# Kernel optimization log

Measured on AMD Instinct MI355X. Metric: run time of the kernel, lower is better.

Reference implementation:

```python
import jax, jax.numpy as jnp
import numpy as np

FEATS = 1024
HEAD = 16
MLP_HIDDEN = 4096
HEAD_DIM = FEATS // HEAD
SQRT_D = float(FEATS) ** 0.5  # module scales by sqrt(feats), not sqrt(head_dim)
LN_EPS = 1e-5


def layer_norm(x, g, b):
    mu = jnp.mean(x, axis=-1, keepdims=True)
    var = jnp.mean(jnp.square(x - mu), axis=-1, keepdims=True)
    return (x - mu) * jax.lax.rsqrt(var + LN_EPS) * g + b


def setup_inputs() -> dict:
    key = jax.random.key(0)
    ks = jax.random.split(key, 12)
    s = 1.0 / np.sqrt(FEATS)
    s2 = 1.0 / np.sqrt(MLP_HIDDEN)
    return {
        "x": jax.random.normal(ks[0], (2, 2048, FEATS), dtype=jnp.float32),
        "ln1_g": jnp.ones((FEATS,), jnp.float32),
        "ln1_b": jnp.zeros((FEATS,), jnp.float32),
        "wq": jax.random.normal(ks[1], (FEATS, FEATS), jnp.float32) * s,
        "bq": jnp.zeros((FEATS,), jnp.float32),
        "wk": jax.random.normal(ks[2], (FEATS, FEATS), jnp.float32) * s,
        "bk": jnp.zeros((FEATS,), jnp.float32),
        "wv": jax.random.normal(ks[3], (FEATS, FEATS), jnp.float32) * s,
        "bv": jnp.zeros((FEATS,), jnp.float32),
        "wo": jax.random.normal(ks[4], (FEATS, FEATS), jnp.float32) * s,
        "bo": jnp.zeros((FEATS,), jnp.float32),
        "ln2_g": jnp.ones((FEATS,), jnp.float32),
        "ln2_b": jnp.zeros((FEATS,), jnp.float32),
        "w1": jax.random.normal(ks[5], (MLP_HIDDEN, FEATS), jnp.float32) * s,
        "b1": jnp.zeros((MLP_HIDDEN,), jnp.float32),
        "w2": jax.random.normal(ks[6], (FEATS, MLP_HIDDEN), jnp.float32) * s2,
        "b2": jnp.zeros((FEATS,), jnp.float32),
    }


def reference(x, ln1_g, ln1_b, wq, bq, wk, bk, wv, bv, wo, bo,
              ln2_g, ln2_b, w1, b1, w2, b2):
    b, n, f = x.shape
    h = layer_norm(x, ln1_g, ln1_b)
    # qkv projections (torch Linear: y = x @ W.T + b)
    q = (h @ wq.T + bq).reshape(b, n, HEAD, HEAD_DIM).transpose(0, 2, 1, 3)
    k = (h @ wk.T + bk).reshape(b, n, HEAD, HEAD_DIM).transpose(0, 2, 1, 3)
    v = (h @ wv.T + bv).reshape(b, n, HEAD, HEAD_DIM).transpose(0, 2, 1, 3)
    score = jax.nn.softmax(jnp.einsum('bhif,bhjf->bhij', q, k) / SQRT_D, axis=-1)
    attn = jnp.einsum('bhij,bhjf->bihf', score, v).reshape(b, n, f)
    o = attn @ wo.T + bo
    out1 = o + x
    h2 = layer_norm(out1, ln2_g, ln2_b)
    mlp = jax.nn.relu(jax.nn.relu(h2 @ w1.T + b1) @ w2.T + b2)
    return mlp + out1
```

## Files before the change

### kernel.cpp

```cpp
#include <hip/hip_runtime.h>
#include <hip/hip_bf16.h>

#define FEATS 1024
#define NH 16
#define HD 64
#define SEQ 2048
#define BATCH 2
#define MTOT (BATCH*SEQ)
#define MLPH 4096

typedef __attribute__((ext_vector_type(8))) short bf16x8;
typedef __attribute__((ext_vector_type(4))) short bf16x4;
typedef __attribute__((ext_vector_type(4))) float f32x4;

static_assert(sizeof(bf16x8) == 16, "bf16x8 must be 16B");

__device__ __forceinline__ unsigned short f2bf(float f) {
    unsigned int u = __float_as_uint(f);
    unsigned int lsb = (u >> 16) & 1u;
    u += 0x7fffu + lsb;
    return (unsigned short)(u >> 16);
}

#define ASYNC16(GP, LP) __builtin_amdgcn_global_load_lds( \
    (const __attribute__((address_space(1))) void*)(GP),  \
    (__attribute__((address_space(3))) void*)(LP), 16, 0, 0)

__global__ __launch_bounds__(256) void cvt_kernel(const float* __restrict__ src,
                                                  unsigned short* __restrict__ dst, int n) {
    int i = (blockIdx.x * 256 + threadIdx.x) * 4;
    if (i + 3 < n) {
        float4 v = *(const float4*)(src + i);
        ushort4 o;
        o.x = f2bf(v.x); o.y = f2bf(v.y); o.z = f2bf(v.z); o.w = f2bf(v.w);
        *(ushort4*)(dst + i) = o;
    }
}

__global__ __launch_bounds__(256) void concat3_kernel(const float* __restrict__ a,
                                                      const float* __restrict__ b,
                                                      const float* __restrict__ c,
                                                      float* __restrict__ o) {
    int i = blockIdx.x * 256 + threadIdx.x;
    float v = (i < 1024) ? a[i] : ((i < 2048) ? b[i - 1024] : c[i - 2048]);
    o[i] = v;
}

__global__ __launch_bounds__(256) void ln_kernel(const float* __restrict__ x,
                                                 const float* __restrict__ g,
                                                 const float* __restrict__ bta,
                                                 unsigned short* __restrict__ h) {
    __shared__ float red[8];
    const int row = blockIdx.x;
    const int t = threadIdx.x;
    const float* xr = x + (size_t)row * FEATS;
    float4 v = ((const float4*)xr)[t];
    float s  = v.x + v.y + v.z + v.w;
    float ss = v.x * v.x + v.y * v.y + v.z * v.z + v.w * v.w;
#pragma unroll
    for (int off = 1; off < 64; off <<= 1) {
        s  += __shfl_xor(s, off);
        ss += __shfl_xor(ss, off);
    }
    const int w = t >> 6;
    if ((t & 63) == 0) { red[w] = s; red[4 + w] = ss; }
    __syncthreads();
    s  = red[0] + red[1] + red[2] + red[3];
    ss = red[4] + red[5] + red[6] + red[7];
    const float mu  = s * (1.f / FEATS);
    const float var = ss * (1.f / FEATS) - mu * mu;
    const float rs  = rsqrtf(var + 1e-5f);
    float4 gv = ((const float4*)g)[t];
    float4 bv = ((const float4*)bta)[t];
    ushort4 ov;
    ov.x = f2bf((v.x - mu) * rs * gv.x + bv.x);
    ov.y = f2bf((v.y - mu) * rs * gv.y + bv.y);
    ov.z = f2bf((v.z - mu) * rs * gv.z + bv.z);
    ov.w = f2bf((v.w - mu) * rs * gv.w + bv.w);
    ((ushort4*)h)[(size_t)row * (FEATS / 4) + t] = ov;
}

template <bool RELU, bool ADD, bool OUTBF16>
__global__ __launch_bounds__(256, 3)
void gemm_kernel(const unsigned short* __restrict__ A,
                 const unsigned short* __restrict__ W,
                 const float* __restrict__ bias,
                 const float* __restrict__ addend,
                 void* __restrict__ outp,
                 int M, int N, int K, int gx) {
    __shared__ unsigned short lds[3][2][128 * 32];

    const int t = threadIdx.x;
    const int w = t >> 6, lane = t & 63;
    const int wr = w >> 1, wc = w & 1;
    const int li = lane & 15, lj = lane >> 4;

    const int nwg = gridDim.x;
    const int cpx = nwg >> 3;
    const int wg = blockIdx.x;
    const int swz = (wg & 7) * cpx + (wg >> 3);
    const int mb = (swz / gx) * 128, nb = (swz % gx) * 128;

    const int srow = lane >> 2, sc = (lane & 3) * 8;
    const unsigned short* gA = A + (size_t)(mb + w * 16 + srow) * K + sc;
    const unsigned short* gB = W + (size_t)(nb + w * 16 + srow) * K + sc;
    const size_t half = (size_t)64 * K;
    const int lbase = w * 512 + lane * 8;

    const int nt = K >> 5;

#define STAGE(BUF, K0)                                             \
    do {                                                           \
        unsigned short* la_ = &lds[BUF][0][lbase];                 \
        unsigned short* lb_ = &lds[BUF][1][lbase];                 \
        ASYNC16(gA + (K0), la_);                                   \
        ASYNC16(gA + half + (K0), la_ + 2048);                     \
        ASYNC16(gB + (K0), lb_);                                   \
        ASYNC16(gB + half + (K0), lb_ + 2048);                     \
    } while (0)

    STAGE(0, 0);
    STAGE(1, 32);
    asm volatile("s_waitcnt vmcnt(4)" ::: "memory");
    __builtin_amdgcn_s_barrier();

    f32x4 acc[4][4] = {};

    for (int i = 0; i < nt; ++i) {
        const int cur = i % 3;
        const unsigned short* Al = &lds[cur][0][0];
        const unsigned short* Bl = &lds[cur][1][0];

        bf16x8 af[4], bfr[4];
#pragma unroll
        for (int m = 0; m < 4; m++)
            af[m] = *(const bf16x8*)(Al + (wr * 64 + m * 16 + li) * 32 + lj * 8);
#pragma unroll
        for (int n = 0; n < 4; n++)
            bfr[n] = *(const bf16x8*)(Bl + (wc * 64 + n * 16 + li) * 32 + lj * 8);

        const int pf = i + 2 < nt;
        if (pf) STAGE((i + 2) % 3, (i + 2) * 32);

#pragma unroll
        for (int m = 0; m < 4; m++)
#pragma unroll
            for (int n = 0; n < 4; n++)
                acc[m][n] = __builtin_amdgcn_mfma_f32_16x16x32_bf16(af[m], bfr[n], acc[m][n], 0, 0, 0);

        if (i + 1 < nt) {
            if (pf) asm volatile("s_waitcnt vmcnt(4)" ::: "memory");
            else    asm volatile("s_waitcnt vmcnt(0)" ::: "memory");
            __builtin_amdgcn_s_barrier();
        }
    }
#undef STAGE

#pragma unroll
    for (int m = 0; m < 4; m++) {
#pragma unroll
        for (int n = 0; n < 4; n++) {
            const int col = nb + wc * 64 + n * 16 + li;
            const float bv = bias[col];
#pragma unroll
            for (int r = 0; r < 4; r++) {
                const int row = mb + wr * 64 + m * 16 + lj * 4 + r;
                float v = acc[m][n][r] + bv;
                if (RELU) v = fmaxf(v, 0.f);
                if (ADD)  v += addend[(size_t)row * N + col];
                if (OUTBF16)
                    ((unsigned short*)outp)[(size_t)row * N + col] = f2bf(v);
                else
                    ((float*)outp)[(size_t)row * N + col] = v;
            }
        }
    }
}

__global__ __launch_bounds__(256) void vtrans_kernel(const unsigned short* __restrict__ qkv,
                                                     unsigned short* __restrict__ vt) {
    constexpr int LDV = 68;
    __shared__ unsigned short Vl[64 * LDV];
    const int bh = blockIdx.x, st = blockIdx.y;
    const int b = bh >> 4, h = bh & 15;
    const int t = threadIdx.x;
    const unsigned short* src = qkv + (size_t)(b * SEQ + st * 64) * (3 * FEATS) + 2 * FEATS + h * HD;
#pragma unroll
    for (int i = 0; i < 2; i++) {
        int idx = t + i * 256;
        int r = idx >> 3, c = (idx & 7) * 8;
        *(bf16x8*)(Vl + r * LDV + c) = *(const bf16x8*)(src + (size_t)r * (3 * FEATS) + c);
    }
    __syncthreads();
    unsigned short* dst = vt + (size_t)bh * HD * SEQ + st * 64;
#pragma unroll
    for (int i = 0; i < 2; i++) {
        int idx = t + i * 256;
        int d = idx >> 3, s8 = (idx & 7) * 8;
        bf16x8 v;
#pragma unroll
        for (int j = 0; j < 8; j++) v[j] = Vl[(s8 + j) * LDV + d];
        *(bf16x8*)(dst + (size_t)d * SEQ + s8) = v;
    }
}

__global__ __launch_bounds__(512, 4)
void attn_kernel(const unsigned short* __restrict__ qkv,
                 const unsigned short* __restrict__ vt,
                 unsigned short* __restrict__ out) {
    constexpr int LK = 72;
    __shared__ unsigned short Kl[2][64 * LK];
    __shared__ unsigned short Vtl[2][64 * LK];

    const int bh = blockIdx.x;
    const int b = bh >> 4, h = bh & 15;
    const int q0 = blockIdx.y * 128;
    const int t = threadIdx.x, w = t >> 6, lane = t & 63;
    const int li = lane & 15, lj = lane >> 4;

    const size_t rstr = 3 * FEATS;
    const unsigned short* qkvb = qkv + (size_t)(b * SEQ) * rstr;
    const unsigned short* ksrc = qkvb + FEATS + h * HD;
    const unsigned short* vsrc = vt + (size_t)bh * HD * SEQ;

    bf16x8 aq[2];
#pragma unroll
    for (int kk = 0; kk < 2; kk++)
        aq[kk] = *(const bf16x8*)(qkvb + (size_t)(q0 + w * 16 + li) * rstr + h * HD + kk * 32 + lj * 8);

    f32x4 o[4] = {};
    float lsum = 0.f;
    const float c2 = 1.4426950408889634f / 32.0f;

    const int sr = t >> 3, scol = (t & 7) * 8;
    const unsigned short* kg = ksrc + (size_t)sr * rstr + scol;
    const unsigned short* vg = vsrc + (size_t)sr * SEQ + scol;
    const int ldoK = sr * LK + scol;
    const int posA = (scol & 32) + ((scol & 8) << 1) + ((scol & 16) >> 2);
    const int ldoV = sr * LK + posA;

    const int nt = SEQ / 64;

    {
        bf16x8 k0 = *(const bf16x8*)kg;
        bf16x8 v0 = *(const bf16x8*)vg;
        *(bf16x8*)(&Kl[0][ldoK]) = k0;
        bf16x4 vlo = __builtin_shufflevector(v0, v0, 0, 1, 2, 3);
        bf16x4 vhi = __builtin_shufflevector(v0, v0, 4, 5, 6, 7);
        *(bf16x4*)(&Vtl[0][ldoV])     = vlo;
        *(bf16x4*)(&Vtl[0][ldoV + 8]) = vhi;
    }

    int cur = 0;
    for (int i = 0; i < nt; ++i) {
        bf16x8 kreg, vreg;
        if (i + 1 < nt) {
            kreg = *(const bf16x8*)(kg + (size_t)(i + 1) * 64 * rstr);
            vreg = *(const bf16x8*)(vg + (i + 1) * 64);
        }

        asm volatile("s_waitcnt lgkmcnt(0)" ::: "memory");
        __builtin_amdgcn_s_barrier();

        const unsigned short* Kc = Kl[cur];
        const unsigned short* Vc = Vtl[cur];

        f32x4 s[4];
        __builtin_amdgcn_s_setprio(1);
#pragma unroll
        for (int n = 0; n < 4; n++) {
            bf16x8 k0 = *(const bf16x8*)(Kc + (n * 16 + li) * LK + lj * 8);
            bf16x8 k1 = *(const bf16x8*)(Kc + (n * 16 + li) * LK + 32 + lj * 8);
            f32x4 acc = {};
            acc = __builtin_amdgcn_mfma_f32_16x16x32_bf16(k0, aq[0], acc, 0, 0, 0);
            acc = __builtin_amdgcn_mfma_f32_16x16x32_bf16(k1, aq[1], acc, 0, 0, 0);
            s[n] = acc;
        }
        __builtin_amdgcn_s_setprio(0);

        float p[4][4];
#pragma unroll
        for (int n = 0; n < 4; n++)
#pragma unroll
            for (int r = 0; r < 4; r++) {
                p[n][r] = exp2f(s[n][r] * c2);
                lsum += p[n][r];
            }
        union { unsigned u[4]; bf16x8 v; } A0u, A1u;
#pragma unroll
        for (int n = 0; n < 2; n++) {
            asm("v_cvt_pk_bf16_f32 %0, %1, %2" : "=v"(A0u.u[n * 2])     : "v"(p[n][0]), "v"(p[n][1]));
            asm("v_cvt_pk_bf16_f32 %0, %1, %2" : "=v"(A0u.u[n * 2 + 1]) : "v"(p[n][2]), "v"(p[n][3]));
            asm("v_cvt_pk_bf16_f32 %0, %1, %2" : "=v"(A1u.u[n * 2])     : "v"(p[n + 2][0]), "v"(p[n + 2][1]));
            asm("v_cvt_pk_bf16_f32 %0, %1, %2" : "=v"(A1u.u[n * 2 + 1]) : "v"(p[n + 2][2]), "v"(p[n + 2][3]));
        }

        __builtin_amdgcn_s_setprio(1);
#pragma unroll
        for (int n = 0; n < 4; n++) {
            bf16x8 bv0 = *(const bf16x8*)(Vc + (n * 16 + li) * LK + lj * 8);
            bf16x8 bv1 = *(const bf16x8*)(Vc + (n * 16 + li) * LK + 32 + lj * 8);
            o[n] = __builtin_amdgcn_mfma_f32_16x16x32_bf16(A0u.v, bv0, o[n], 0, 0, 0);
            o[n] = __builtin_amdgcn_mfma_f32_16x16x32_bf16(A1u.v, bv1, o[n], 0, 0, 0);
        }
        __builtin_amdgcn_s_setprio(0);

        if (i + 1 < nt) {
            *(bf16x8*)(&Kl[cur ^ 1][ldoK]) = kreg;
            bf16x4 vlo = __builtin_shufflevector(vreg, vreg, 0, 1, 2, 3);
            bf16x4 vhi = __builtin_shufflevector(vreg, vreg, 4, 5, 6, 7);
            *(bf16x4*)(&Vtl[cur ^ 1][ldoV])     = vlo;
            *(bf16x4*)(&Vtl[cur ^ 1][ldoV + 8]) = vhi;
        }
        cur ^= 1;
    }

    lsum += __shfl_xor(lsum, 16);
    lsum += __shfl_xor(lsum, 32);
    const float dinv = 1.f / lsum;
    float inv[4];
#pragma unroll
    for (int r = 0; r < 4; r++)
        inv[r] = __shfl(dinv, lj * 4 + r);

    unsigned short* ob = out + (size_t)(b * SEQ + q0 + w * 16) * FEATS + h * HD;
#pragma unroll
    for (int n = 0; n < 4; n++)
#pragma unroll
        for (int r = 0; r < 4; r++)
            ob[(size_t)(lj * 4 + r) * FEATS + n * 16 + li] = f2bf(o[n][r] * inv[r]);
}

extern "C" void kernel_launch(void* const* d_in, const int* in_sizes, int n_in,
                              void* d_out, int out_size, void* d_ws, size_t ws_size,
                              hipStream_t stream) {
    const float* x     = (const float*)d_in[0];
    const float* ln1_g = (const float*)d_in[1];
    const float* ln1_b = (const float*)d_in[2];
    const float* wq    = (const float*)d_in[3];
    const float* bq    = (const float*)d_in[4];
    const float* wk    = (const float*)d_in[5];
    const float* bk    = (const float*)d_in[6];
    const float* wv    = (const float*)d_in[7];
    const float* bvv   = (const float*)d_in[8];
    const float* wo    = (const float*)d_in[9];
    const float* bo    = (const float*)d_in[10];
    const float* ln2_g = (const float*)d_in[11];
    const float* ln2_b = (const float*)d_in[12];
    const float* w1    = (const float*)d_in[13];
    const float* b1    = (const float*)d_in[14];
    const float* w2    = (const float*)d_in[15];
    const float* b2    = (const float*)d_in[16];

    unsigned short* wqkv_b = (unsigned short*)d_ws;
    unsigned short* wo_b   = wqkv_b + 3072 * 1024;
    unsigned short* w1_b   = wo_b + 1024 * 1024;
    unsigned short* w2_b   = w1_b + 4096 * 1024;
    float*          bqkv   = (float*)(w2_b + 1024 * 4096);
    unsigned short* region = (unsigned short*)(bqkv + 3072);
    unsigned short* qkvb   = region;
    unsigned short* hb     = region + (size_t)4096 * 3072;
    unsigned short* vtb    = hb;
    unsigned short* a1     = region;
    unsigned short* attn_o = region + (size_t)4096 * 4096;
    unsigned short* h2     = attn_o;
    float*          out1   = (float*)(attn_o + (size_t)4096 * 1024);
    float*          outf   = (float*)d_out;

    dim3 blk(256);

    cvt_kernel<<<1024, blk, 0, stream>>>(wq, wqkv_b, 1024 * 1024);
    cvt_kernel<<<1024, blk, 0, stream>>>(wk, wqkv_b + 1024 * 1024, 1024 * 1024);
    cvt_kernel<<<1024, blk, 0, stream>>>(wv, wqkv_b + 2 * 1024 * 1024, 1024 * 1024);
    cvt_kernel<<<1024, blk, 0, stream>>>(wo, wo_b, 1024 * 1024);
    cvt_kernel<<<4096, blk, 0, stream>>>(w1, w1_b, 4096 * 1024);
    cvt_kernel<<<4096, blk, 0, stream>>>(w2, w2_b, 4096 * 1024);
    concat3_kernel<<<12, blk, 0, stream>>>(bq, bk, bvv, bqkv);

    ln_kernel<<<MTOT, blk, 0, stream>>>(x, ln1_g, ln1_b, hb);

    gemm_kernel<false, false, true><<<768, blk, 0, stream>>>(
        hb, wqkv_b, bqkv, nullptr, qkvb, MTOT, 3072, FEATS, 24);

    vtrans_kernel<<<dim3(BATCH * NH, SEQ / 64), blk, 0, stream>>>(qkvb, vtb);

    attn_kernel<<<dim3(BATCH * NH, SEQ / 128), dim3(512), 0, stream>>>(qkvb, vtb, attn_o);

    gemm_kernel<false, true, false><<<256, blk, 0, stream>>>(
        attn_o, wo_b, bo, x, out1, MTOT, FEATS, FEATS, 8);

    ln_kernel<<<MTOT, blk, 0, stream>>>(out1, ln2_g, ln2_b, h2);

    gemm_kernel<true, false, true><<<1024, blk, 0, stream>>>(
        h2, w1_b, b1, nullptr, a1, MTOT, MLPH, FEATS, 32);

    gemm_kernel<true, true, false><<<256, blk, 0, stream>>>(
        a1, w2_b, b2, out1, outf, MTOT, FEATS, MLPH, 8);
}
```

Baseline: 249.4 us.

## Widen attention key tile to 128 and fold softmax scale into Q weights

The attention kernel now processes 128 keys per iteration instead of 64, which halves the number of loop iterations and barriers and issues larger loads per thread. The V-transpose LDS layout is widened to match. The softmax scale (log2e/sqrt(1024)) is folded into the Q weight and bias conversion, so the per-element multiply before exp2 goes away. The grid is also transposed so that consecutive blocks share the same head. In exchange, LDS use and register pressure grow, which may limit occupancy, and rounding Q to bf16 after scaling shifts the numerics slightly.

```diff
diff --git a/kernel.cpp b/kernel.cpp
--- a/kernel.cpp
+++ b/kernel.cpp
@@ -8,6 +8,7 @@
 #define BATCH 2
 #define MTOT (BATCH*SEQ)
 #define MLPH 4096
+#define QSCALE 0.04508422277369218f
 
 typedef __attribute__((ext_vector_type(8))) short bf16x8;
 typedef __attribute__((ext_vector_type(4))) short bf16x4;
@@ -27,12 +28,14 @@
     (__attribute__((address_space(3))) void*)(LP), 16, 0, 0)
 
 __global__ __launch_bounds__(256) void cvt_kernel(const float* __restrict__ src,
-                                                  unsigned short* __restrict__ dst, int n) {
+                                                  unsigned short* __restrict__ dst,
+                                                  int n, float scale) {
     int i = (blockIdx.x * 256 + threadIdx.x) * 4;
     if (i + 3 < n) {
         float4 v = *(const float4*)(src + i);
         ushort4 o;
-        o.x = f2bf(v.x); o.y = f2bf(v.y); o.z = f2bf(v.z); o.w = f2bf(v.w);
+        o.x = f2bf(v.x * scale); o.y = f2bf(v.y * scale);
+        o.z = f2bf(v.z * scale); o.w = f2bf(v.w * scale);
         *(ushort4*)(dst + i) = o;
     }
 }
@@ -42,7 +45,7 @@
                                                       const float* __restrict__ c,
                                                       float* __restrict__ o) {
     int i = blockIdx.x * 256 + threadIdx.x;
-    float v = (i < 1024) ? a[i] : ((i < 2048) ? b[i - 1024] : c[i - 2048]);
+    float v = (i < 1024) ? a[i] * QSCALE : ((i < 2048) ? b[i - 1024] : c[i - 2048]);
     o[i] = v;
 }
 
@@ -209,12 +212,13 @@
                  const unsigned short* __restrict__ vt,
                  unsigned short* __restrict__ out) {
     constexpr int LK = 72;
-    __shared__ unsigned short Kl[2][64 * LK];
-    __shared__ unsigned short Vtl[2][64 * LK];
-
-    const int bh = blockIdx.x;
+    constexpr int LV = 136;
+    __shared__ unsigned short Kl[2][128 * LK];
+    __shared__ unsigned short Vtl[2][64 * LV];
+
+    const int bh = blockIdx.y;
     const int b = bh >> 4, h = bh & 15;
-    const int q0 = blockIdx.y * 128;
+    const int q0 = blockIdx.x * 128;
     const int t = threadIdx.x, w = t >> 6, lane = t & 63;
     const int li = lane & 15, lj = lane >> 4;
 
@@ -230,33 +234,45 @@
 
     f32x4 o[4] = {};
     float lsum = 0.f;
-    const float c2 = 1.4426950408889634f / 32.0f;
-
-    const int sr = t >> 3, scol = (t & 7) * 8;
-    const unsigned short* kg = ksrc + (size_t)sr * rstr + scol;
-    const unsigned short* vg = vsrc + (size_t)sr * SEQ + scol;
-    const int ldoK = sr * LK + scol;
-    const int posA = (scol & 32) + ((scol & 8) << 1) + ((scol & 16) >> 2);
-    const int ldoV = sr * LK + posA;
-
-    const int nt = SEQ / 64;
+
+    const int skey = t >> 2, sc = (t & 3) * 16;
+    const unsigned short* kg = ksrc + (size_t)skey * rstr + sc;
+    const int ldoK = skey * LK + sc;
+    const int sd = t >> 3, c0 = (t & 7) * 16;
+    const unsigned short* vg = vsrc + (size_t)sd * SEQ + c0;
+    const int posA = (c0 & 96) | (((c0 >> 2) & 3) << 3) | (((c0 >> 4) & 1) << 2);
+    const int ldoV = sd * LV + posA;
+
+    const int nt = SEQ / 128;
+
+#define VSPLIT(VR0, VR1, BUF)                                            \
+    do {                                                                 \
+        *(bf16x4*)(&Vtl[BUF][ldoV])      = __builtin_shufflevector(VR0, VR0, 0, 1, 2, 3); \
+        *(bf16x4*)(&Vtl[BUF][ldoV + 8])  = __builtin_shufflevector(VR0, VR0, 4, 5, 6, 7); \
+        *(bf16x4*)(&Vtl[BUF][ldoV + 16]) = __builtin_shufflevector(VR1, VR1, 0, 1, 2, 3); \
+        *(bf16x4*)(&Vtl[BUF][ldoV + 24]) = __builtin_shufflevector(VR1, VR1, 4, 5, 6, 7); \
+    } while (0)
 
     {
         bf16x8 k0 = *(const bf16x8*)kg;
+        bf16x8 k1 = *(const bf16x8*)(kg + 8);
         bf16x8 v0 = *(const bf16x8*)vg;
-        *(bf16x8*)(&Kl[0][ldoK]) = k0;
-        bf16x4 vlo = __builtin_shufflevector(v0, v0, 0, 1, 2, 3);
-        bf16x4 vhi = __builtin_shufflevector(v0, v0, 4, 5, 6, 7);
-        *(bf16x4*)(&Vtl[0][ldoV])     = vlo;
-        *(bf16x4*)(&Vtl[0][ldoV + 8]) = vhi;
+        bf16x8 v1 = *(const bf16x8*)(vg + 8);
+        *(bf16x8*)(&Kl[0][ldoK])     = k0;
+        *(bf16x8*)(&Kl[0][ldoK + 8]) = k1;
+        VSPLIT(v0, v1, 0);
     }
 
     int cur = 0;
     for (int i = 0; i < nt; ++i) {
-        bf16x8 kreg, vreg;
+        bf16x8 kr0, kr1, vr0, vr1;
         if (i + 1 < nt) {
-            kreg = *(const bf16x8*)(kg + (size_t)(i + 1) * 64 * rstr);
-            vreg = *(const bf16x8*)(vg + (i + 1) * 64);
+            const unsigned short* kn = kg + (size_t)(i + 1) * 128 * rstr;
+            const unsigned short* vn = vg + (i + 1) * 128;
+            kr0 = *(const bf16x8*)kn;
+            kr1 = *(const bf16x8*)(kn + 8);
+            vr0 = *(const bf16x8*)vn;
+            vr1 = *(const bf16x8*)(vn + 8);
         }
 
         asm volatile("s_waitcnt lgkmcnt(0)" ::: "memory");
@@ -265,10 +281,10 @@
         const unsigned short* Kc = Kl[cur];
         const unsigned short* Vc = Vtl[cur];
 
-        f32x4 s[4];
+        f32x4 s[8];
         __builtin_amdgcn_s_setprio(1);
 #pragma unroll
-        for (int n = 0; n < 4; n++) {
+        for (int n = 0; n < 8; n++) {
             bf16x8 k0 = *(const bf16x8*)(Kc + (n * 16 + li) * LK + lj * 8);
             bf16x8 k1 = *(const bf16x8*)(Kc + (n * 16 + li) * LK + 32 + lj * 8);
             f32x4 acc = {};
@@ -278,42 +294,43 @@
         }
         __builtin_amdgcn_s_setprio(0);
 
-        float p[4][4];
-#pragma unroll
-        for (int n = 0; n < 4; n++)
+        bf16x8 A[4];
+#pragma unroll
+        for (int kk = 0; kk < 4; kk++) {
+            float p[8];
 #pragma unroll
             for (int r = 0; r < 4; r++) {
-                p[n][r] = exp2f(s[n][r] * c2);
-                lsum += p[n][r];
+                p[r]     = exp2f(s[2 * kk][r]);
+                p[4 + r] = exp2f(s[2 * kk + 1][r]);
+                lsum += p[r] + p[4 + r];
             }
-        union { unsigned u[4]; bf16x8 v; } A0u, A1u;
-#pragma unroll
-        for (int n = 0; n < 2; n++) {
-            asm("v_cvt_pk_bf16_f32 %0, %1, %2" : "=v"(A0u.u[n * 2])     : "v"(p[n][0]), "v"(p[n][1]));
-            asm("v_cvt_pk_bf16_f32 %0, %1, %2" : "=v"(A0u.u[n * 2 + 1]) : "v"(p[n][2]), "v"(p[n][3]));
-            asm("v_cvt_pk_bf16_f32 %0, %1, %2" : "=v"(A1u.u[n * 2])     : "v"(p[n + 2][0]), "v"(p[n + 2][1]));
-            asm("v_cvt_pk_bf16_f32 %0, %1, %2" : "=v"(A1u.u[n * 2 + 1]) : "v"(p[n + 2][2]), "v"(p[n + 2][3]));
+            union { unsigned u[4]; bf16x8 v; } Au;
+            asm("v_cvt_pk_bf16_f32 %0, %1, %2" : "=v"(Au.u[0]) : "v"(p[0]), "v"(p[1]));
+            asm("v_cvt_pk_bf16_f32 %0, %1, %2" : "=v"(Au.u[1]) : "v"(p[2]), "v"(p[3]));
+            asm("v_cvt_pk_bf16_f32 %0, %1, %2" : "=v"(Au.u[2]) : "v"(p[4]), "v"(p[5]));
+            asm("v_cvt_pk_bf16_f32 %0, %1, %2" : "=v"(Au.u[3]) : "v"(p[6]), "v"(p[7]));
+            A[kk] = Au.v;
         }
 
         __builtin_amdgcn_s_setprio(1);
 #pragma unroll
         for (int n = 0; n < 4; n++) {
-            bf16x8 bv0 = *(const bf16x8*)(Vc + (n * 16 + li) * LK + lj * 8);
-            bf16x8 bv1 = *(const bf16x8*)(Vc + (n * 16 + li) * LK + 32 + lj * 8);
-            o[n] = __builtin_amdgcn_mfma_f32_16x16x32_bf16(A0u.v, bv0, o[n], 0, 0, 0);
-            o[n] = __builtin_amdgcn_mfma_f32_16x16x32_bf16(A1u.v, bv1, o[n], 0, 0, 0);
+#pragma unroll
+            for (int kk = 0; kk < 4; kk++) {
+                bf16x8 bv = *(const bf16x8*)(Vc + (n * 16 + li) * LV + kk * 32 + lj * 8);
+                o[n] = __builtin_amdgcn_mfma_f32_16x16x32_bf16(A[kk], bv, o[n], 0, 0, 0);
+            }
         }
         __builtin_amdgcn_s_setprio(0);
 
         if (i + 1 < nt) {
-            *(bf16x8*)(&Kl[cur ^ 1][ldoK]) = kreg;
-            bf16x4 vlo = __builtin_shufflevector(vreg, vreg, 0, 1, 2, 3);
-            bf16x4 vhi = __builtin_shufflevector(vreg, vreg, 4, 5, 6, 7);
-            *(bf16x4*)(&Vtl[cur ^ 1][ldoV])     = vlo;
-            *(bf16x4*)(&Vtl[cur ^ 1][ldoV + 8]) = vhi;
+            *(bf16x8*)(&Kl[cur ^ 1][ldoK])     = kr0;
+            *(bf16x8*)(&Kl[cur ^ 1][ldoK + 8]) = kr1;
+            VSPLIT(vr0, vr1, cur ^ 1);
         }
         cur ^= 1;
     }
+#undef VSPLIT
 
     lsum += __shfl_xor(lsum, 16);
     lsum += __shfl_xor(lsum, 32);
@@ -369,12 +386,12 @@
 
     dim3 blk(256);
 
-    cvt_kernel<<<1024, blk, 0, stream>>>(wq, wqkv_b, 1024 * 1024);
-    cvt_kernel<<<1024, blk, 0, stream>>>(wk, wqkv_b + 1024 * 1024, 1024 * 1024);
-    cvt_kernel<<<1024, blk, 0, stream>>>(wv, wqkv_b + 2 * 1024 * 1024, 1024 * 1024);
-    cvt_kernel<<<1024, blk, 0, stream>>>(wo, wo_b, 1024 * 1024);
-    cvt_kernel<<<4096, blk, 0, stream>>>(w1, w1_b, 4096 * 1024);
-    cvt_kernel<<<4096, blk, 0, stream>>>(w2, w2_b, 4096 * 1024);
+    cvt_kernel<<<1024, blk, 0, stream>>>(wq, wqkv_b, 1024 * 1024, QSCALE);
+    cvt_kernel<<<1024, blk, 0, stream>>>(wk, wqkv_b + 1024 * 1024, 1024 * 1024, 1.0f);
+    cvt_kernel<<<1024, blk, 0, stream>>>(wv, wqkv_b + 2 * 1024 * 1024, 1024 * 1024, 1.0f);
+    cvt_kernel<<<1024, blk, 0, stream>>>(wo, wo_b, 1024 * 1024, 1.0f);
+    cvt_kernel<<<4096, blk, 0, stream>>>(w1, w1_b, 4096 * 1024, 1.0f);
+    cvt_kernel<<<4096, blk, 0, stream>>>(w2, w2_b, 4096 * 1024, 1.0f);
     concat3_kernel<<<12, blk, 0, stream>>>(bq, bk, bvv, bqkv);
 
     ln_kernel<<<MTOT, blk, 0, stream>>>(x, ln1_g, ln1_b, hb);
@@ -384,7 +401,7 @@
 
     vtrans_kernel<<<dim3(BATCH * NH, SEQ / 64), blk, 0, stream>>>(qkvb, vtb);
 
-    attn_kernel<<<dim3(BATCH * NH, SEQ / 128), dim3(512), 0, stream>>>(qkvb, vtb, attn_o);
+    attn_kernel<<<dim3(SEQ / 128, BATCH * NH), dim3(512), 0, stream>>>(qkvb, vtb, attn_o);
 
     gemm_kernel<false, true, false><<<256, blk, 0, stream>>>(
         attn_o, wo_b, bo, x, out1, MTOT, FEATS, FEATS, 8);
```

Result: no change. 247.6 us (-0.7%).
